# Performance work log

Measured on AMD Instinct MI355X. Metric: run time of the kernel, lower is better.

Reference implementation:

```python
import jax, jax.numpy as jnp
import numpy as np
import math

D_SINGLE, D_PAIR, H, PQ, PV = 384, 128, 12, 4, 8
DH = D_SINGLE // H
OUT_DIM = H * DH + H * PV * 4 + H * D_PAIR


def setup_inputs() -> dict:
    key = jax.random.key(0)
    ks = jax.random.split(key, 24)
    B, L = 1, 512
    inp = {
        'single': jax.random.normal(ks[0], (B, L, D_SINGLE), jnp.float32),
        'pair': jax.random.normal(ks[1], (B, L, L, D_PAIR), jnp.float32),
        'rot_mats': jax.random.normal(ks[2], (B, L, 3, 3), jnp.float32),
        'trans': jax.random.normal(ks[3], (B, L, 3), jnp.float32),
        'mask': jnp.ones((B, L), jnp.float32),
        'ln_w': jnp.ones((D_SINGLE,), jnp.float32),
        'ln_b': jnp.zeros((D_SINGLE,), jnp.float32),
        'Wq': jax.random.normal(ks[4], (D_SINGLE, H * DH), jnp.float32) * 0.02,
        'bq': jnp.zeros((H * DH,), jnp.float32),
        'Wk': jax.random.normal(ks[5], (D_SINGLE, H * DH), jnp.float32) * 0.02,
        'bk': jnp.zeros((H * DH,), jnp.float32),
        'Wv': jax.random.normal(ks[6], (D_SINGLE, H * DH), jnp.float32) * 0.02,
        'bv': jnp.zeros((H * DH,), jnp.float32),
        'Wqp': jax.random.normal(ks[7], (D_SINGLE, H * PQ * 3), jnp.float32) * 0.02,
        'bqp': jnp.zeros((H * PQ * 3,), jnp.float32),
        'Wkp': jax.random.normal(ks[8], (D_SINGLE, H * PQ * 3), jnp.float32) * 0.02,
        'bkp': jnp.zeros((H * PQ * 3,), jnp.float32),
        'Wvp': jax.random.normal(ks[9], (D_SINGLE, H * PV * 3), jnp.float32) * 0.02,
        'bvp': jnp.zeros((H * PV * 3,), jnp.float32),
        'Wpb': jax.random.normal(ks[10], (D_PAIR, H), jnp.float32) * 0.02,
        'bpb': jnp.zeros((H,), jnp.float32),
        'Wo': jax.random.normal(ks[11], (OUT_DIM, D_SINGLE), jnp.float32) * 0.02,
        'bo': jnp.zeros((D_SINGLE,), jnp.float32),
        'w_c': jnp.asarray(1.0 / math.sqrt(3.0), jnp.float32),
        'w_l': jnp.asarray(1.0 / 3.0, jnp.float32),
        'gamma_h': jnp.ones((H,), jnp.float32),
    }
    return inp


def _layer_norm(x, w, b, eps=1e-5):
    mu = jnp.mean(x, axis=-1, keepdims=True)
    var = jnp.mean((x - mu) ** 2, axis=-1, keepdims=True)
    return (x - mu) * jax.lax.rsqrt(var + eps) * w + b


def reference(single, pair, rot_mats, trans, mask, ln_w, ln_b, Wq, bq, Wk, bk, Wv, bv,
              Wqp, bqp, Wkp, bkp, Wvp, bvp, Wpb, bpb, Wo, bo, w_c, w_l, gamma_h):
    B, L, _ = single.shape
    sn = _layer_norm(single, ln_w, ln_b)
    q = (sn @ Wq + bq).reshape(B, L, H, DH)
    k = (sn @ Wk + bk).reshape(B, L, H, DH)
    v = (sn @ Wv + bv).reshape(B, L, H, DH)
    qp = (sn @ Wqp + bqp).reshape(B, L, H, PQ, 3)
    kp = (sn @ Wkp + bkp).reshape(B, L, H, PQ, 3)
    vp = (sn @ Wvp + bvp).reshape(B, L, H, PV, 3)

    t = trans[:, :, None, None, :]  # [B,L,1,1,3]
    qg = jnp.einsum('blij,blhpj->blhpi', rot_mats, qp) + t
    kg = jnp.einsum('blij,blhpj->blhpi', rot_mats, kp) + t
    vg = jnp.einsum('blij,blhpj->blhpi', rot_mats, vp) + t

    # sequence logits [B,H,L,L]
    seq_logits = jnp.einsum('bihd,bjhd->bhij', q, k) * w_c / math.sqrt(DH)

    # geometric logits: pairwise point distances [B,H,L,L]
    q_pts = jnp.transpose(qg, (0, 2, 1, 3, 4))  # [B,H,L,PQ,3]
    k_pts = jnp.transpose(kg, (0, 2, 1, 3, 4))
    diff = q_pts[:, :, :, None] - k_pts[:, :, None]  # [B,H,L,L,PQ,3]
    dist_sq = jnp.sum(diff ** 2, axis=-1)            # [B,H,L,L,PQ]
    geo_logits = -0.5 * jnp.sum(dist_sq, axis=-1) * gamma_h[None, :, None, None] * w_l

    pair_bias = jnp.transpose(pair @ Wpb + bpb, (0, 3, 1, 2))  # [B,H,L,L]
    logits = seq_logits + geo_logits + pair_bias

    mask_2d = (mask[:, :, None] * mask[:, None, :])[:, None]  # [B,1,L,L]
    logits = jnp.where(mask_2d > 0, logits, jnp.float32(-1e9))
    attn = jax.nn.softmax(logits, axis=-1)  # [B,H,L,L]

    # sequence aggregation -> [B,L,H,DH]
    seq_out = jnp.einsum('bhij,bjhd->bihd', attn, v).reshape(B, L, H * DH)

    # point aggregation -> local frame features
    pts_out = jnp.einsum('bhij,bjhpd->bihpd', attn, vg)  # [B,L,H,PV,3]
    pts_local = jnp.einsum('blji,blhpj->blhpi', rot_mats, pts_out - t)
    pts_norm = jnp.linalg.norm(pts_local, axis=-1, keepdims=True)
    pts_feat = jnp.concatenate([pts_norm, pts_local], axis=-1).reshape(B, L, H * PV * 4)

    # pair aggregation -> [B,L,H*D_PAIR]
    pair_out = jnp.einsum('bhij,bijd->bihd', attn, pair).reshape(B, L, H * D_PAIR)

    combined = jnp.concatenate([seq_out, pts_feat, pair_out], axis=-1)
    return combined @ Wo + bo
```

## Files before the change

### kernel.cpp

```cpp
#include <hip/hip_runtime.h>
#include <math.h>

#define LQ    512
#define DS    384
#define DPAIR 128
#define NH    12
#define NPP   1792
#define FE    48
#define TJC   64
#define NC    8

__global__ void k_concat_w(const float* __restrict__ Wq, const float* __restrict__ Wk,
                           const float* __restrict__ Wv, const float* __restrict__ Wqp,
                           const float* __restrict__ Wkp, const float* __restrict__ Wvp,
                           const float* __restrict__ bq, const float* __restrict__ bk,
                           const float* __restrict__ bv, const float* __restrict__ bqp,
                           const float* __restrict__ bkp, const float* __restrict__ bvp,
                           const float* __restrict__ Wpb,
                           float* __restrict__ Wcat, float* __restrict__ bcat,
                           float* __restrict__ WpbT) {
  int idx = blockIdx.x * 256 + threadIdx.x;
  const int total = DS * NPP;
  if (idx < total) {
    int k = idx / NPP, c = idx % NPP;
    float v = 0.f;
    if (c < 384)       v = Wq[k*384 + c];
    else if (c < 768)  v = Wk[k*384 + c-384];
    else if (c < 1152) v = Wv[k*384 + c-768];
    else if (c < 1296) v = Wqp[k*144 + c-1152];
    else if (c < 1440) v = Wkp[k*144 + c-1296];
    else if (c < 1728) v = Wvp[k*288 + c-1440];
    Wcat[idx] = v;
  } else if (idx < total + NPP) {
    int c = idx - total;
    float v = 0.f;
    if (c < 384)       v = bq[c];
    else if (c < 768)  v = bk[c-384];
    else if (c < 1152) v = bv[c-768];
    else if (c < 1296) v = bqp[c-1152];
    else if (c < 1440) v = bkp[c-1296];
    else if (c < 1728) v = bvp[c-1440];
    bcat[c] = v;
  } else if (idx < total + NPP + DPAIR*NH) {
    int e = idx - total - NPP;
    int k = e / NH, h = e % NH;
    WpbT[h*DPAIR + k] = Wpb[e];
  }
}

__global__ __launch_bounds__(128) void k_layernorm(const float* __restrict__ x,
                                                   const float* __restrict__ w,
                                                   const float* __restrict__ b,
                                                   float* __restrict__ y) {
  __shared__ float red[128];
  __shared__ float s_mu, s_rstd;
  int i = blockIdx.x, t = threadIdx.x;
  float v0 = x[i*DS + t], v1 = x[i*DS + t + 128], v2 = x[i*DS + t + 256];
  red[t] = v0 + v1 + v2; __syncthreads();
  for (int s = 64; s > 0; s >>= 1) { if (t < s) red[t] += red[t+s]; __syncthreads(); }
  if (t == 0) s_mu = red[0] * (1.f/384.f);
  __syncthreads();
  float mu = s_mu;
  float d0 = v0-mu, d1 = v1-mu, d2 = v2-mu;
  red[t] = d0*d0 + d1*d1 + d2*d2; __syncthreads();
  for (int s = 64; s > 0; s >>= 1) { if (t < s) red[t] += red[t+s]; __syncthreads(); }
  if (t == 0) s_rstd = rsqrtf(red[0] * (1.f/384.f) + 1e-5f);
  __syncthreads();
  float r = s_rstd;
  y[i*DS + t      ] = d0*r*w[t      ] + b[t      ];
  y[i*DS + t + 128] = d1*r*w[t + 128] + b[t + 128];
  y[i*DS + t + 256] = d2*r*w[t + 256] + b[t + 256];
}

__global__ __launch_bounds__(256) void k_gemm_nn(const float* __restrict__ A,
                                                 const float* __restrict__ B,
                                                 const float* __restrict__ bias,
                                                 float* __restrict__ C,
                                                 float* __restrict__ Cpart,
                                                 int M, int N, int K) {
  __shared__ float As[16*68];
  __shared__ float Bs[16*68];
  int t = threadIdx.x;
  int mg = t >> 4, ng = t & 15;
  int i0 = blockIdx.y * 64, j0 = blockIdx.x * 64;
  int KS = gridDim.z;
  int kper = K / KS;
  int kbeg = blockIdx.z * kper;
  float acc[4][4] = {};
  for (int k0 = kbeg; k0 < kbeg + kper; k0 += 16) {
    int e = t;
    #pragma unroll
    for (int s = 0; s < 4; s++, e += 256) {
      int m = e >> 4, k = e & 15;
      As[k*68 + m] = A[(size_t)(i0+m)*K + k0 + k];
      int k2 = e >> 6, n = e & 63;
      Bs[k2*68 + n] = B[(size_t)(k0+k2)*N + j0 + n];
    }
    __syncthreads();
    #pragma unroll
    for (int k = 0; k < 16; k++) {
      float4 av = *(const float4*)(As + k*68 + mg*4);
      float4 bv = *(const float4*)(Bs + k*68 + ng*4);
      float a[4] = {av.x, av.y, av.z, av.w};
      float b[4] = {bv.x, bv.y, bv.z, bv.w};
      #pragma unroll
      for (int y = 0; y < 4; y++)
        #pragma unroll
        for (int x = 0; x < 4; x++)
          acc[y][x] = fmaf(a[y], b[x], acc[y][x]);
    }
    __syncthreads();
  }
  if (KS == 1) {
    #pragma unroll
    for (int y = 0; y < 4; y++) {
      int m = i0 + mg*4 + y;
      #pragma unroll
      for (int x = 0; x < 4; x++) {
        int n = j0 + ng*4 + x;
        C[(size_t)m*N + n] = acc[y][x] + bias[n];
      }
    }
  } else {
    float* dst = Cpart + (size_t)blockIdx.z * M * N;
    #pragma unroll
    for (int y = 0; y < 4; y++) {
      int m = i0 + mg*4 + y;
      #pragma unroll
      for (int x = 0; x < 4; x++) {
        int n = j0 + ng*4 + x;
        dst[(size_t)m*N + n] = acc[y][x];
      }
    }
  }
}

__global__ void k_reduce_bias(const float* __restrict__ part, const float* __restrict__ bias,
                              float* __restrict__ out, int MN, int N, int KS) {
  int e = blockIdx.x * 256 + threadIdx.x;
  if (e >= MN) return;
  float s = bias[e % N];
  for (int z = 0; z < KS; z++) s += part[(size_t)z*MN + e];
  out[e] = s;
}

__global__ void k_rotfeat(const float* __restrict__ C1, const float* __restrict__ rot,
                          const float* __restrict__ trans, const float* __restrict__ gamma,
                          const float* __restrict__ w_c, const float* __restrict__ w_l,
                          float* __restrict__ Af, float* __restrict__ Bf,
                          float* __restrict__ vgb) {
  int idx = blockIdx.x * 256 + threadIdx.x;
  if (idx >= LQ*NH) return;
  int h = idx % NH, i = idx / NH;
  float R[9], tr[3];
  #pragma unroll
  for (int r = 0; r < 9; r++) R[r] = rot[(size_t)i*9 + r];
  #pragma unroll
  for (int r = 0; r < 3; r++) tr[r] = trans[(size_t)i*3 + r];

  float s  = w_c[0] * rsqrtf(32.f);
  float gp = gamma[h] * w_l[0];
  float* a  = Af + ((size_t)h*LQ + i)*FE;
  float* bb = Bf + ((size_t)h*LQ + i)*FE;
  const float* q = C1 + (size_t)i*NPP + h*32;
  const float* k = C1 + (size_t)i*NPP + 384 + h*32;
  #pragma unroll 8
  for (int d = 0; d < 32; d++) { a[d] = s*q[d]; bb[d] = k[d]; }

  const float* qp = C1 + (size_t)i*NPP + 1152 + h*12;
  const float* kp = C1 + (size_t)i*NPP + 1296 + h*12;
  float sq = 0.f, sk = 0.f;
  #pragma unroll
  for (int p = 0; p < 4; p++) {
    float x = qp[p*3], y = qp[p*3+1], z = qp[p*3+2];
    #pragma unroll
    for (int r = 0; r < 3; r++) {
      float g = fmaf(R[r*3],x, fmaf(R[r*3+1],y, fmaf(R[r*3+2],z, tr[r])));
      a[32 + p*3 + r] = gp*g;
      sq = fmaf(g,g,sq);
    }
    float xk = kp[p*3], yk = kp[p*3+1], zk = kp[p*3+2];
    #pragma unroll
    for (int r = 0; r < 3; r++) {
      float g = fmaf(R[r*3],xk, fmaf(R[r*3+1],yk, fmaf(R[r*3+2],zk, tr[r])));
      bb[32 + p*3 + r] = g;
      sk = fmaf(g,g,sk);
    }
  }
  a[44] = -0.5f*gp*sq; a[45] = 1.f; a[46] = 0.f; a[47] = 0.f;
  bb[44] = 1.f; bb[45] = -0.5f*gp*sk; bb[46] = 0.f; bb[47] = 0.f;

  const float* vp = C1 + (size_t)i*NPP + 1440 + h*24;
  float* vd = vgb + ((size_t)i*NH + h)*24;
  #pragma unroll
  for (int p = 0; p < 8; p++) {
    float x = vp[p*3], y = vp[p*3+1], z = vp[p*3+2];
    #pragma unroll
    for (int r = 0; r < 3; r++)
      vd[p*3 + r] = fmaf(R[r*3],x, fmaf(R[r*3+1],y, fmaf(R[r*3+2],z, tr[r])));
  }
}

__global__ __launch_bounds__(256) void k_logits_nt(const float* __restrict__ Af,
                                                   const float* __restrict__ Bf,
                                                   float* __restrict__ S) {
  __shared__ float As[48*68];
  __shared__ float Bs[48*68];
  int h = blockIdx.z;
  int i0 = blockIdx.y * 64, j0 = blockIdx.x * 64;
  int t = threadIdx.x;
  int mg = t >> 4, ng = t & 15;
  const float* Ah = Af + (size_t)h*LQ*FE;
  const float* Bh = Bf + (size_t)h*LQ*FE;
  for (int e = t; e < 64*48; e += 256) {
    int m = e / 48, k = e % 48;
    As[k*68 + m] = Ah[(size_t)(i0+m)*FE + k];
    Bs[k*68 + m] = Bh[(size_t)(j0+m)*FE + k];
  }
  __syncthreads();
  float acc[4][4] = {};
  #pragma unroll 8
  for (int k = 0; k < 48; k++) {
    float4 av = *(const float4*)(As + k*68 + mg*4);
    float4 bv = *(const float4*)(Bs + k*68 + ng*4);
    float a[4] = {av.x, av.y, av.z, av.w};
    float b[4] = {bv.x, bv.y, bv.z, bv.w};
    #pragma unroll
    for (int y = 0; y < 4; y++)
      #pragma unroll
      for (int x = 0; x < 4; x++)
        acc[y][x] = fmaf(a[y], b[x], acc[y][x]);
  }
  #pragma unroll
  for (int y = 0; y < 4; y++) {
    #pragma unroll
    for (int x = 0; x < 4; x++)
      S[((size_t)h*LQ + i0 + mg*4 + y)*LQ + j0 + ng*4 + x] = acc[y][x];
  }
}

__global__ __launch_bounds__(256, 2) void k_pair_chunk(
    const float* __restrict__ pair, const float* __restrict__ WpbT,
    const float* __restrict__ bpb, const float* __restrict__ mask,
    float* __restrict__ S, float* __restrict__ pairpart, float* __restrict__ msum) {
  __shared__ float tile[TJC*133];
  __shared__ float wt[NH*TJC];
  int i = blockIdx.x, c = blockIdx.y, t = threadIdx.x;
  int j0 = c*TJC;

  const float4* src = (const float4*)(pair + ((size_t)i*LQ + j0)*DPAIR);
  #pragma unroll
  for (int u = 0; u < 8; u++) {
    int e = t + u*256; int row = e >> 5, c4 = e & 31;
    *(float4*)&tile[row*133 + c4*4] = src[e];
  }

  int j = t & 63;
  int hg = __builtin_amdgcn_readfirstlane(t >> 6);
  int h0 = hg*3;
  float l[3];
  #pragma unroll
  for (int q = 0; q < 3; q++)
    l[q] = S[((size_t)(h0+q)*LQ + i)*LQ + j0 + j] + bpb[h0+q];
  bool dead = (mask[i] * mask[j0 + j] <= 0.f);
  __syncthreads();

  {
    const float* w0p = WpbT + (size_t)(h0+0)*DPAIR;
    const float* w1p = WpbT + (size_t)(h0+1)*DPAIR;
    const float* w2p = WpbT + (size_t)(h0+2)*DPAIR;
    float a0 = 0.f, a1 = 0.f, a2 = 0.f;
    #pragma unroll 8
    for (int k = 0; k < DPAIR; k += 4) {
      float4 pv = *(const float4*)&tile[j*133 + k];
      float4 w0 = *(const float4*)(w0p + k);
      float4 w1 = *(const float4*)(w1p + k);
      float4 w2 = *(const float4*)(w2p + k);
      a0 = fmaf(pv.x,w0.x, fmaf(pv.y,w0.y, fmaf(pv.z,w0.z, fmaf(pv.w,w0.w, a0))));
      a1 = fmaf(pv.x,w1.x, fmaf(pv.y,w1.y, fmaf(pv.z,w1.z, fmaf(pv.w,w1.w, a1))));
      a2 = fmaf(pv.x,w2.x, fmaf(pv.y,w2.y, fmaf(pv.z,w2.z, fmaf(pv.w,w2.w, a2))));
    }
    l[0] += a0; l[1] += a1; l[2] += a2;
    if (dead) { l[0] = -1e9f; l[1] = -1e9f; l[2] = -1e9f; }
  }

  #pragma unroll
  for (int q = 0; q < 3; q++) {
    float m = l[q];
    #pragma unroll
    for (int o = 32; o > 0; o >>= 1) m = fmaxf(m, __shfl_xor(m, o, 64));
    float w = __expf(l[q] - m);
    float sm = w;
    #pragma unroll
    for (int o = 32; o > 0; o >>= 1) sm += __shfl_xor(sm, o, 64);
    wt[(h0+q)*TJC + j] = w;
    S[((size_t)(h0+q)*LQ + i)*LQ + j0 + j] = w;
    if (j == 0) {
      float* dst = msum + (((size_t)i*NC + c)*NH + h0 + q)*2;
      dst[0] = m; dst[1] = sm;
    }
  }
  __syncthreads();

  int dg = t & 31, strip = t >> 5, jb = strip*8;
  float4 pv[8];
  #pragma unroll
  for (int q = 0; q < 8; q++) pv[q] = *(const float4*)&tile[(jb+q)*133 + dg*4];
  float4 acc[NH];
  #pragma unroll
  for (int h = 0; h < NH; h++) acc[h] = make_float4(0.f,0.f,0.f,0.f);
  #pragma unroll
  for (int h = 0; h < NH; h++) {
    float4 w0 = *(const float4*)&wt[h*TJC + jb];
    float4 w1 = *(const float4*)&wt[h*TJC + jb + 4];
    float wq[8] = {w0.x,w0.y,w0.z,w0.w,w1.x,w1.y,w1.z,w1.w};
    float4 a = acc[h];
    #pragma unroll
    for (int q = 0; q < 8; q++) {
      a.x = fmaf(wq[q], pv[q].x, a.x);
      a.y = fmaf(wq[q], pv[q].y, a.y);
      a.z = fmaf(wq[q], pv[q].z, a.z);
      a.w = fmaf(wq[q], pv[q].w, a.w);
    }
    acc[h] = a;
  }
  __syncthreads();

  float4* red4 = (float4*)tile;
  float4 tot[2];
  tot[0] = make_float4(0.f,0.f,0.f,0.f);
  tot[1] = make_float4(0.f,0.f,0.f,0.f);
  #pragma unroll
  for (int half = 0; half < 2; half++) {
    if ((strip >> 2) == half) {
      #pragma unroll
      for (int h = 0; h < NH; h++)
        red4[(((strip & 3)*NH) + h)*32 + dg] = acc[h];
    }
    __syncthreads();
    for (int e = t, u = 0; e < NH*32; e += 256, u++) {
      int rh = e >> 5, rd = e & 31;
      #pragma unroll
      for (int s4 = 0; s4 < 4; s4++) {
        float4 v = red4[((s4*NH) + rh)*32 + rd];
        tot[u].x += v.x; tot[u].y += v.y; tot[u].z += v.z; tot[u].w += v.w;
      }
    }
    __syncthreads();
  }
  for (int e = t, u = 0; e < NH*32; e += 256, u++) {
    int rh = e >> 5, rd = e & 31;
    *(float4*)&pairpart[(((size_t)i*NC + c)*NH + rh)*DPAIR + rd*4] = tot[u];
  }
}

__global__ __launch_bounds__(384) void k_scs_pairout(
    const float* __restrict__ msum, const float* __restrict__ pairpart,
    float* __restrict__ scs_g, float* __restrict__ comb) {
  __shared__ float scs[NH*NC];
  int i = blockIdx.x, t = threadIdx.x;
  if (t < NH) {
    float m = -3.0e38f;
    float mc[NC], sc_[NC];
    #pragma unroll
    for (int c = 0; c < NC; c++) {
      const float* p = msum + (((size_t)i*NC + c)*NH + t)*2;
      mc[c] = p[0]; sc_[c] = p[1];
      m = fmaxf(m, mc[c]);
    }
    float s = 0.f;
    #pragma unroll
    for (int c = 0; c < NC; c++) s += sc_[c] * __expf(mc[c] - m);
    float inv = 1.f / s;
    #pragma unroll
    for (int c = 0; c < NC; c++) {
      float v = __expf(mc[c] - m) * inv;
      scs[t*NC + c] = v;
      scs_g[((size_t)i*NH + t)*NC + c] = v;
    }
  }
  __syncthreads();
  int h = t >> 5, d = t & 31;
  float4 tot = make_float4(0.f,0.f,0.f,0.f);
  #pragma unroll
  for (int c = 0; c < NC; c++) {
    float sc = scs[h*NC + c];
    float4 v = *(const float4*)&pairpart[(((size_t)i*NC + c)*NH + h)*DPAIR + d*4];
    tot.x = fmaf(v.x, sc, tot.x); tot.y = fmaf(v.y, sc, tot.y);
    tot.z = fmaf(v.z, sc, tot.z); tot.w = fmaf(v.w, sc, tot.w);
  }
  *(float4*)&comb[(size_t)i*2304 + 768 + h*DPAIR + d*4] = tot;
}

__global__ __launch_bounds__(256) void k_attn_v(const float* __restrict__ attn,
                                                const float* __restrict__ C1,
                                                const float* __restrict__ vg,
                                                const float* __restrict__ scs,
                                                float* __restrict__ psum) {
  __shared__ float As[64*68];
  __shared__ float Vs[64*68];
  int i0 = blockIdx.x * 64;
  int h = blockIdx.y;
  int z = blockIdx.z;
  int t = threadIdx.x;
  int mg = t >> 4, ng = t & 15;
  float acc[4][4] = {};
  for (int k0 = z*128; k0 < z*128 + 128; k0 += 64) {
    int c = k0 >> 6;
    __syncthreads();
    for (int e = t; e < 64*64; e += 256) {
      int m = e >> 6, j = e & 63;
      float sc = scs[((size_t)(i0+m)*NH + h)*NC + c];
      As[j*68 + m] = attn[((size_t)h*LQ + i0 + m)*LQ + k0 + j] * sc;
    }
    for (int e = t; e < 64*64; e += 256) {
      int j = e >> 6, cc = e & 63;
      float v = 0.f;
      if (cc < 32)      v = C1[(size_t)(k0+j)*NPP + 768 + h*32 + cc];
      else if (cc < 56) v = vg[((size_t)(k0+j)*NH + h)*24 + (cc-32)];
      Vs[j*68 + cc] = v;
    }
    __syncthreads();
    #pragma unroll 4
    for (int j = 0; j < 64; j++) {
      float4 av = *(const float4*)(As + j*68 + mg*4);
      float4 bv = *(const float4*)(Vs + j*68 + ng*4);
      float a[4] = {av.x, av.y, av.z, av.w};
      float b[4] = {bv.x, bv.y, bv.z, bv.w};
      #pragma unroll
      for (int y = 0; y < 4; y++)
        #pragma unroll
        for (int x = 0; x < 4; x++)
          acc[y][x] = fmaf(a[y], b[x], acc[y][x]);
    }
  }
  #pragma unroll
  for (int y = 0; y < 4; y++) {
    int i = i0 + mg*4 + y;
    #pragma unroll
    for (int x = 0; x < 4; x++) {
      int n = ng*4 + x;
      psum[(((size_t)z*LQ + i)*NH + h)*64 + n] = acc[y][x];
    }
  }
}

__global__ void k_avpts(const float* __restrict__ psum, const float* __restrict__ rot,
                        const float* __restrict__ trans, float* __restrict__ comb) {
  int idx = blockIdx.x * 256 + threadIdx.x;
  if (idx >= LQ*NH*40) return;
  int w = idx % 40; int ih = idx / 40; int h = ih % NH; int i = ih / NH;
  size_t base = ((size_t)i*NH + h)*64;
  if (w < 32) {
    float s = 0.f;
    for (int z = 0; z < 4; z++) s += psum[(size_t)z*LQ*NH*64 + base + w];
    comb[(size_t)i*2304 + h*32 + w] = s;
  } else {
    int p = w - 32;
    float g[3];
    #pragma unroll
    for (int r = 0; r < 3; r++) {
      int n = 32 + p*3 + r;
      float s = 0.f;
      for (int z = 0; z < 4; z++) s += psum[(size_t)z*LQ*NH*64 + base + n];
      g[r] = s;
    }
    const float* R = rot + (size_t)i*9;
    const float* tr = trans + (size_t)i*3;
    float x = g[0]-tr[0], y = g[1]-tr[1], z = g[2]-tr[2];
    float lx = fmaf(R[0],x, fmaf(R[3],y, R[6]*z));
    float ly = fmaf(R[1],x, fmaf(R[4],y, R[7]*z));
    float lz = fmaf(R[2],x, fmaf(R[5],y, R[8]*z));
    float nrm = sqrtf(fmaf(lx,lx, fmaf(ly,ly, lz*lz)));
    float* dst = comb + (size_t)i*2304 + 384 + (h*8 + p)*4;
    dst[0] = nrm; dst[1] = lx; dst[2] = ly; dst[3] = lz;
  }
}

extern "C" void kernel_launch(void* const* d_in, const int* in_sizes, int n_in,
                              void* d_out, int out_size, void* d_ws, size_t ws_size,
                              hipStream_t stream) {
  const float* single = (const float*)d_in[0];
  const float* pair   = (const float*)d_in[1];
  const float* rot    = (const float*)d_in[2];
  const float* trans  = (const float*)d_in[3];
  const float* mask   = (const float*)d_in[4];
  const float* ln_w   = (const float*)d_in[5];
  const float* ln_b   = (const float*)d_in[6];
  const float* Wq     = (const float*)d_in[7];
  const float* bq     = (const float*)d_in[8];
  const float* Wk     = (const float*)d_in[9];
  const float* bk     = (const float*)d_in[10];
  const float* Wv     = (const float*)d_in[11];
  const float* bv     = (const float*)d_in[12];
  const float* Wqp    = (const float*)d_in[13];
  const float* bqp    = (const float*)d_in[14];
  const float* Wkp    = (const float*)d_in[15];
  const float* bkp    = (const float*)d_in[16];
  const float* Wvp    = (const float*)d_in[17];
  const float* bvp    = (const float*)d_in[18];
  const float* Wpb    = (const float*)d_in[19];
  const float* bpb    = (const float*)d_in[20];
  const float* Wo     = (const float*)d_in[21];
  const float* bo     = (const float*)d_in[22];
  const float* w_c    = (const float*)d_in[23];
  const float* w_l    = (const float*)d_in[24];
  const float* gamma  = (const float*)d_in[25];
  float* out = (float*)d_out;

  float* p = (float*)d_ws;
  auto alloc = [&](size_t n) { float* r = p; p += n; return r; };
  float* Wcat    = alloc((size_t)DS*NPP);
  float* bcat    = alloc(NPP);
  float* WpbT    = alloc((size_t)NH*DPAIR);
  float* sn      = alloc((size_t)LQ*DS);
  float* C1      = alloc((size_t)LQ*NPP);
  float* vgb     = alloc((size_t)LQ*NH*24);
  float* Af      = alloc((size_t)NH*LQ*FE);
  float* Bf      = alloc((size_t)NH*LQ*FE);
  float* S       = alloc((size_t)NH*LQ*LQ);
  float* pairpart= alloc((size_t)LQ*NC*NH*DPAIR);
  float* msum    = alloc((size_t)LQ*NC*NH*2);
  float* scs_g   = alloc((size_t)LQ*NH*NC);
  float* comb    = alloc((size_t)LQ*2304);
  float* scratch = alloc((size_t)2*LQ*NPP);

  k_concat_w<<<dim3((DS*NPP + NPP + DPAIR*NH + 255)/256), 256, 0, stream>>>(
      Wq, Wk, Wv, Wqp, Wkp, Wvp, bq, bk, bv, bqp, bkp, bvp, Wpb, Wcat, bcat, WpbT);
  k_layernorm<<<dim3(LQ), 128, 0, stream>>>(single, ln_w, ln_b, sn);
  k_gemm_nn<<<dim3(NPP/64, LQ/64, 2), 256, 0, stream>>>(sn, Wcat, nullptr, nullptr, scratch, LQ, NPP, DS);
  k_reduce_bias<<<dim3((LQ*NPP + 255)/256), 256, 0, stream>>>(scratch, bcat, C1, LQ*NPP, NPP, 2);
  k_rotfeat<<<dim3((LQ*NH + 255)/256), 256, 0, stream>>>(C1, rot, trans, gamma, w_c, w_l, Af, Bf, vgb);
  k_logits_nt<<<dim3(LQ/64, LQ/64, NH), 256, 0, stream>>>(Af, Bf, S);
  k_pair_chunk<<<dim3(LQ, NC), 256, 0, stream>>>(pair, WpbT, bpb, mask, S, pairpart, msum);
  k_scs_pairout<<<dim3(LQ), 384, 0, stream>>>(msum, pairpart, scs_g, comb);
  k_attn_v<<<dim3(LQ/64, NH, 4), 256, 0, stream>>>(S, C1, vgb, scs_g, scratch);
  k_avpts<<<dim3((LQ*NH*40 + 255)/256), 256, 0, stream>>>(scratch, rot, trans, comb);
  k_gemm_nn<<<dim3(DS/64, LQ/64, 8), 256, 0, stream>>>(comb, Wo, nullptr, nullptr, scratch, LQ, DS, 2304);
  k_reduce_bias<<<dim3((LQ*DS + 255)/256), 256, 0, stream>>>(scratch, bo, out, LQ*DS, DS, 8);
}
```

Measured before the change: 377.1 us.

## Run projection and output GEMMs on MFMA with split-bf16 emulated fp32

```diff
diff --git a/kernel.cpp b/kernel.cpp
--- a/kernel.cpp
+++ b/kernel.cpp
@@ -10,48 +10,116 @@
 #define TJC   64
 #define NC    8
 
-__global__ void k_concat_w(const float* __restrict__ Wq, const float* __restrict__ Wk,
-                           const float* __restrict__ Wv, const float* __restrict__ Wqp,
-                           const float* __restrict__ Wkp, const float* __restrict__ Wvp,
-                           const float* __restrict__ bq, const float* __restrict__ bk,
-                           const float* __restrict__ bv, const float* __restrict__ bqp,
-                           const float* __restrict__ bkp, const float* __restrict__ bvp,
-                           const float* __restrict__ Wpb,
-                           float* __restrict__ Wcat, float* __restrict__ bcat,
-                           float* __restrict__ WpbT) {
-  int idx = blockIdx.x * 256 + threadIdx.x;
-  const int total = DS * NPP;
-  if (idx < total) {
-    int k = idx / NPP, c = idx % NPP;
-    float v = 0.f;
-    if (c < 384)       v = Wq[k*384 + c];
-    else if (c < 768)  v = Wk[k*384 + c-384];
-    else if (c < 1152) v = Wv[k*384 + c-768];
-    else if (c < 1296) v = Wqp[k*144 + c-1152];
-    else if (c < 1440) v = Wkp[k*144 + c-1296];
-    else if (c < 1728) v = Wvp[k*288 + c-1440];
-    Wcat[idx] = v;
-  } else if (idx < total + NPP) {
-    int c = idx - total;
-    float v = 0.f;
-    if (c < 384)       v = bq[c];
-    else if (c < 768)  v = bk[c-384];
-    else if (c < 1152) v = bv[c-768];
-    else if (c < 1296) v = bqp[c-1152];
-    else if (c < 1440) v = bkp[c-1296];
-    else if (c < 1728) v = bvp[c-1440];
-    bcat[c] = v;
-  } else if (idx < total + NPP + DPAIR*NH) {
-    int e = idx - total - NPP;
-    int k = e / NH, h = e % NH;
-    WpbT[h*DPAIR + k] = Wpb[e];
-  }
+typedef unsigned short u16;
+typedef unsigned int   u32;
+typedef __attribute__((ext_vector_type(8))) short bf16x8;
+typedef __attribute__((ext_vector_type(4))) float f32x4;
+
+__device__ inline u16 bf16_rne(float x) {
+  u32 u = __float_as_uint(x);
+  u32 r = (u + 0x7FFFu + ((u >> 16) & 1u)) >> 16;
+  return (u16)r;
+}
+__device__ inline void split_bf16(float x, u16& h, u16& l) {
+  u16 hb = bf16_rne(x);
+  float hf = __uint_as_float(((u32)hb) << 16);
+  h = hb;
+  l = bf16_rne(x - hf);
+}
+
+__global__ __launch_bounds__(256) void k_concat_wT(
+    const float* __restrict__ Wq, const float* __restrict__ Wk,
+    const float* __restrict__ Wv, const float* __restrict__ Wqp,
+    const float* __restrict__ Wkp, const float* __restrict__ Wvp,
+    const float* __restrict__ bq, const float* __restrict__ bk,
+    const float* __restrict__ bv, const float* __restrict__ bqp,
+    const float* __restrict__ bkp, const float* __restrict__ bvp,
+    const float* __restrict__ Wpb,
+    u16* __restrict__ Wth, u16* __restrict__ Wtl,
+    float* __restrict__ bcat, float* __restrict__ WpbT) {
+  int blk = blockIdx.x, t = threadIdx.x;
+  if (blk < 168) {
+    __shared__ u16 hi[64][66], lo[64][66];
+    int kb = blk / 28, cb = blk % 28;
+    int k0 = kb * 64, c0 = cb * 64;
+    for (int e = t; e < 4096; e += 256) {
+      int rr = e >> 6, cc = e & 63;
+      int k = k0 + rr, c = c0 + cc;
+      float v = 0.f;
+      if (c < 384)       v = Wq[k*384 + c];
+      else if (c < 768)  v = Wk[k*384 + c-384];
+      else if (c < 1152) v = Wv[k*384 + c-768];
+      else if (c < 1296) v = Wqp[k*144 + c-1152];
+      else if (c < 1440) v = Wkp[k*144 + c-1296];
+      else if (c < 1728) v = Wvp[k*288 + c-1440];
+      u16 h_, l_; split_bf16(v, h_, l_);
+      hi[rr][cc] = h_; lo[rr][cc] = l_;
+    }
+    __syncthreads();
+    for (int e = t; e < 4096; e += 256) {
+      int cc = e >> 6, kk = e & 63;
+      Wth[(size_t)(c0+cc)*DS + k0 + kk] = hi[kk][cc];
+      Wtl[(size_t)(c0+cc)*DS + k0 + kk] = lo[kk][cc];
+    }
+  } else {
+    for (int e = t; e < NPP + NH*DPAIR; e += 256) {
+      if (e < NPP) {
+        int c = e;
+        float v = 0.f;
+        if (c < 384)       v = bq[c];
+        else if (c < 768)  v = bk[c-384];
+        else if (c < 1152) v = bv[c-768];
+        else if (c < 1296) v = bqp[c-1152];
+        else if (c < 1440) v = bkp[c-1296];
+        else if (c < 1728) v = bvp[c-1440];
+        bcat[c] = v;
+      } else {
+        int e2 = e - NPP;
+        int k = e2 / NH, h = e2 % NH;
+        WpbT[h*DPAIR + k] = Wpb[e2];
+      }
+    }
+  }
+}
+
+__global__ __launch_bounds__(256) void k_transpose_split(
+    const float* __restrict__ src, u16* __restrict__ dh, u16* __restrict__ dl,
+    int R, int Cc) {
+  __shared__ u16 hi[64][66], lo[64][66];
+  int r0 = blockIdx.x * 64, c0 = blockIdx.y * 64, t = threadIdx.x;
+  for (int e = t; e < 4096; e += 256) {
+    int rr = e >> 6, cc = e & 63;
+    float v = src[(size_t)(r0+rr)*Cc + c0 + cc];
+    u16 h_, l_; split_bf16(v, h_, l_);
+    hi[rr][cc] = h_; lo[rr][cc] = l_;
+  }
+  __syncthreads();
+  for (int e = t; e < 4096; e += 256) {
+    int cc = e >> 6, rr = e & 63;
+    dh[(size_t)(c0+cc)*R + r0 + rr] = hi[rr][cc];
+    dl[(size_t)(c0+cc)*R + r0 + rr] = lo[rr][cc];
+  }
+}
+
+__global__ void k_split4(const float* __restrict__ src, u16* __restrict__ h,
+                         u16* __restrict__ l, int n4) {
+  int e = blockIdx.x * 256 + threadIdx.x;
+  if (e >= n4) return;
+  float4 v = ((const float4*)src)[e];
+  u16 h0,l0,h1,l1,h2,l2,h3,l3;
+  split_bf16(v.x, h0, l0); split_bf16(v.y, h1, l1);
+  split_bf16(v.z, h2, l2); split_bf16(v.w, h3, l3);
+  uint2 hp, lp;
+  hp.x = (u32)h0 | ((u32)h1 << 16); hp.y = (u32)h2 | ((u32)h3 << 16);
+  lp.x = (u32)l0 | ((u32)l1 << 16); lp.y = (u32)l2 | ((u32)l3 << 16);
+  ((uint2*)h)[e] = hp; ((uint2*)l)[e] = lp;
 }
 
 __global__ __launch_bounds__(128) void k_layernorm(const float* __restrict__ x,
                                                    const float* __restrict__ w,
                                                    const float* __restrict__ b,
-                                                   float* __restrict__ y) {
+                                                   u16* __restrict__ yh,
+                                                   u16* __restrict__ yl) {
   __shared__ float red[128];
   __shared__ float s_mu, s_rstd;
   int i = blockIdx.x, t = threadIdx.x;
@@ -67,70 +135,84 @@
   if (t == 0) s_rstd = rsqrtf(red[0] * (1.f/384.f) + 1e-5f);
   __syncthreads();
   float r = s_rstd;
-  y[i*DS + t      ] = d0*r*w[t      ] + b[t      ];
-  y[i*DS + t + 128] = d1*r*w[t + 128] + b[t + 128];
-  y[i*DS + t + 256] = d2*r*w[t + 256] + b[t + 256];
-}
-
-__global__ __launch_bounds__(256) void k_gemm_nn(const float* __restrict__ A,
-                                                 const float* __restrict__ B,
-                                                 const float* __restrict__ bias,
-                                                 float* __restrict__ C,
-                                                 float* __restrict__ Cpart,
-                                                 int M, int N, int K) {
-  __shared__ float As[16*68];
-  __shared__ float Bs[16*68];
+  float y0 = d0*r*w[t      ] + b[t      ];
+  float y1 = d1*r*w[t + 128] + b[t + 128];
+  float y2 = d2*r*w[t + 256] + b[t + 256];
+  u16 h_, l_;
+  split_bf16(y0, h_, l_); yh[i*DS + t      ] = h_; yl[i*DS + t      ] = l_;
+  split_bf16(y1, h_, l_); yh[i*DS + t + 128] = h_; yl[i*DS + t + 128] = l_;
+  split_bf16(y2, h_, l_); yh[i*DS + t + 256] = h_; yl[i*DS + t + 256] = l_;
+}
+
+__global__ __launch_bounds__(256) void k_gemm_mfma(
+    const u16* __restrict__ Ah, const u16* __restrict__ Al,
+    const u16* __restrict__ Bth, const u16* __restrict__ Btl,
+    const float* __restrict__ bias, float* __restrict__ C,
+    float* __restrict__ Cpart, int M, int N, int K) {
   int t = threadIdx.x;
-  int mg = t >> 4, ng = t & 15;
-  int i0 = blockIdx.y * 64, j0 = blockIdx.x * 64;
+  int lane = t & 63, wave = t >> 6;
+  int wr = wave >> 1, wc = wave & 1;
+  int i0 = blockIdx.y * 64 + wr * 32;
+  int j0 = blockIdx.x * 64 + wc * 32;
   int KS = gridDim.z;
   int kper = K / KS;
-  int kbeg = blockIdx.z * kper;
-  float acc[4][4] = {};
-  for (int k0 = kbeg; k0 < kbeg + kper; k0 += 16) {
-    int e = t;
-    #pragma unroll
-    for (int s = 0; s < 4; s++, e += 256) {
-      int m = e >> 4, k = e & 15;
-      As[k*68 + m] = A[(size_t)(i0+m)*K + k0 + k];
-      int k2 = e >> 6, n = e & 63;
-      Bs[k2*68 + n] = B[(size_t)(k0+k2)*N + j0 + n];
-    }
-    __syncthreads();
-    #pragma unroll
-    for (int k = 0; k < 16; k++) {
-      float4 av = *(const float4*)(As + k*68 + mg*4);
-      float4 bv = *(const float4*)(Bs + k*68 + ng*4);
-      float a[4] = {av.x, av.y, av.z, av.w};
-      float b[4] = {bv.x, bv.y, bv.z, bv.w};
-      #pragma unroll
-      for (int y = 0; y < 4; y++)
-        #pragma unroll
-        for (int x = 0; x < 4; x++)
-          acc[y][x] = fmaf(a[y], b[x], acc[y][x]);
-    }
-    __syncthreads();
-  }
+  size_t kbeg = (size_t)blockIdx.z * kper;
+  int lr = lane & 15, lk = (lane >> 4) << 3;
+
+  const u16* a0h = Ah  + (size_t)(i0 + lr) * K + kbeg + lk;
+  const u16* a1h = a0h + (size_t)16 * K;
+  const u16* a0l = Al  + (size_t)(i0 + lr) * K + kbeg + lk;
+  const u16* a1l = a0l + (size_t)16 * K;
+  const u16* b0h = Bth + (size_t)(j0 + lr) * K + kbeg + lk;
+  const u16* b1h = b0h + (size_t)16 * K;
+  const u16* b0l = Btl + (size_t)(j0 + lr) * K + kbeg + lk;
+  const u16* b1l = b0l + (size_t)16 * K;
+
+  f32x4 c00 = {0.f,0.f,0.f,0.f}, c01 = c00, c10 = c00, c11 = c00;
+  for (int k = 0; k < kper; k += 32) {
+    bf16x8 A0h = *(const bf16x8*)(a0h + k);
+    bf16x8 A1h = *(const bf16x8*)(a1h + k);
+    bf16x8 B0h = *(const bf16x8*)(b0h + k);
+    bf16x8 B1h = *(const bf16x8*)(b1h + k);
+    bf16x8 A0l = *(const bf16x8*)(a0l + k);
+    bf16x8 A1l = *(const bf16x8*)(a1l + k);
+    bf16x8 B0l = *(const bf16x8*)(b0l + k);
+    bf16x8 B1l = *(const bf16x8*)(b1l + k);
+    c00 = __builtin_amdgcn_mfma_f32_16x16x32_bf16(A0h, B0h, c00, 0, 0, 0);
+    c01 = __builtin_amdgcn_mfma_f32_16x16x32_bf16(A0h, B1h, c01, 0, 0, 0);
+    c10 = __builtin_amdgcn_mfma_f32_16x16x32_bf16(A1h, B0h, c10, 0, 0, 0);
+    c11 = __builtin_amdgcn_mfma_f32_16x16x32_bf16(A1h, B1h, c11, 0, 0, 0);
+    c00 = __builtin_amdgcn_mfma_f32_16x16x32_bf16(A0h, B0l, c00, 0, 0, 0);
+    c01 = __builtin_amdgcn_mfma_f32_16x16x32_bf16(A0h, B1l, c01, 0, 0, 0);
+    c10 = __builtin_amdgcn_mfma_f32_16x16x32_bf16(A1h, B0l, c10, 0, 0, 0);
+    c11 = __builtin_amdgcn_mfma_f32_16x16x32_bf16(A1h, B1l, c11, 0, 0, 0);
+    c00 = __builtin_amdgcn_mfma_f32_16x16x32_bf16(A0l, B0h, c00, 0, 0, 0);
+    c01 = __builtin_amdgcn_mfma_f32_16x16x32_bf16(A0l, B1h, c01, 0, 0, 0);
+    c10 = __builtin_amdgcn_mfma_f32_16x16x32_bf16(A1l, B0h, c10, 0, 0, 0);
+    c11 = __builtin_amdgcn_mfma_f32_16x16x32_bf16(A1l, B1h, c11, 0, 0, 0);
+  }
+
+  int orow = (lane >> 4) << 2;
+  int col0 = j0 + lr, col1 = j0 + 16 + lr;
   if (KS == 1) {
-    #pragma unroll
-    for (int y = 0; y < 4; y++) {
-      int m = i0 + mg*4 + y;
-      #pragma unroll
-      for (int x = 0; x < 4; x++) {
-        int n = j0 + ng*4 + x;
-        C[(size_t)m*N + n] = acc[y][x] + bias[n];
-      }
+    float bb0 = bias[col0], bb1 = bias[col1];
+    #pragma unroll
+    for (int r = 0; r < 4; r++) {
+      int row0 = i0 + orow + r, row1 = row0 + 16;
+      C[(size_t)row0*N + col0] = c00[r] + bb0;
+      C[(size_t)row0*N + col1] = c01[r] + bb1;
+      C[(size_t)row1*N + col0] = c10[r] + bb0;
+      C[(size_t)row1*N + col1] = c11[r] + bb1;
     }
   } else {
     float* dst = Cpart + (size_t)blockIdx.z * M * N;
     #pragma unroll
-    for (int y = 0; y < 4; y++) {
-      int m = i0 + mg*4 + y;
-      #pragma unroll
-      for (int x = 0; x < 4; x++) {
-        int n = j0 + ng*4 + x;
-        dst[(size_t)m*N + n] = acc[y][x];
-      }
+    for (int r = 0; r < 4; r++) {
+      int row0 = i0 + orow + r, row1 = row0 + 16;
+      dst[(size_t)row0*N + col0] = c00[r];
+      dst[(size_t)row0*N + col1] = c01[r];
+      dst[(size_t)row1*N + col0] = c10[r];
+      dst[(size_t)row1*N + col1] = c11[r];
     }
   }
 }
@@ -210,12 +292,12 @@
   int i0 = blockIdx.y * 64, j0 = blockIdx.x * 64;
   int t = threadIdx.x;
   int mg = t >> 4, ng = t & 15;
-  const float* Ah = Af + (size_t)h*LQ*FE;
-  const float* Bh = Bf + (size_t)h*LQ*FE;
+  const float* Ahp = Af + (size_t)h*LQ*FE;
+  const float* Bhp = Bf + (size_t)h*LQ*FE;
   for (int e = t; e < 64*48; e += 256) {
     int m = e / 48, k = e % 48;
-    As[k*68 + m] = Ah[(size_t)(i0+m)*FE + k];
-    Bs[k*68 + m] = Bh[(size_t)(j0+m)*FE + k];
+    As[k*68 + m] = Ahp[(size_t)(i0+m)*FE + k];
+    Bs[k*68 + m] = Bhp[(size_t)(j0+m)*FE + k];
   }
   __syncthreads();
   float acc[4][4] = {};
@@ -510,10 +592,16 @@
 
   float* p = (float*)d_ws;
   auto alloc = [&](size_t n) { float* r = p; p += n; return r; };
-  float* Wcat    = alloc((size_t)DS*NPP);
+  u16* WcatTh = (u16*)alloc((size_t)NPP*DS/2);
+  u16* WcatTl = (u16*)alloc((size_t)NPP*DS/2);
+  u16* snh    = (u16*)alloc((size_t)LQ*DS/2);
+  u16* snl    = (u16*)alloc((size_t)LQ*DS/2);
+  u16* WoTh   = (u16*)alloc((size_t)DS*2304/2);
+  u16* WoTl   = (u16*)alloc((size_t)DS*2304/2);
+  u16* combh  = (u16*)alloc((size_t)LQ*2304/2);
+  u16* combl  = (u16*)alloc((size_t)LQ*2304/2);
   float* bcat    = alloc(NPP);
   float* WpbT    = alloc((size_t)NH*DPAIR);
-  float* sn      = alloc((size_t)LQ*DS);
   float* C1      = alloc((size_t)LQ*NPP);
   float* vgb     = alloc((size_t)LQ*NH*24);
   float* Af      = alloc((size_t)NH*LQ*FE);
@@ -525,17 +613,21 @@
   float* comb    = alloc((size_t)LQ*2304);
   float* scratch = alloc((size_t)2*LQ*NPP);
 
-  k_concat_w<<<dim3((DS*NPP + NPP + DPAIR*NH + 255)/256), 256, 0, stream>>>(
-      Wq, Wk, Wv, Wqp, Wkp, Wvp, bq, bk, bv, bqp, bkp, bvp, Wpb, Wcat, bcat, WpbT);
-  k_layernorm<<<dim3(LQ), 128, 0, stream>>>(single, ln_w, ln_b, sn);
-  k_gemm_nn<<<dim3(NPP/64, LQ/64, 2), 256, 0, stream>>>(sn, Wcat, nullptr, nullptr, scratch, LQ, NPP, DS);
-  k_reduce_bias<<<dim3((LQ*NPP + 255)/256), 256, 0, stream>>>(scratch, bcat, C1, LQ*NPP, NPP, 2);
+  k_concat_wT<<<dim3(169), 256, 0, stream>>>(
+      Wq, Wk, Wv, Wqp, Wkp, Wvp, bq, bk, bv, bqp, bkp, bvp, Wpb,
+      WcatTh, WcatTl, bcat, WpbT);
+  k_transpose_split<<<dim3(2304/64, DS/64), 256, 0, stream>>>(Wo, WoTh, WoTl, 2304, DS);
+  k_layernorm<<<dim3(LQ), 128, 0, stream>>>(single, ln_w, ln_b, snh, snl);
+  k_gemm_mfma<<<dim3(NPP/64, LQ/64, 1), 256, 0, stream>>>(
+      snh, snl, WcatTh, WcatTl, bcat, C1, nullptr, LQ, NPP, DS);
   k_rotfeat<<<dim3((LQ*NH + 255)/256), 256, 0, stream>>>(C1, rot, trans, gamma, w_c, w_l, Af, Bf, vgb);
   k_logits_nt<<<dim3(LQ/64, LQ/64, NH), 256, 0, stream>>>(Af, Bf, S);
   k_pair_chunk<<<dim3(LQ, NC), 256, 0, stream>>>(pair, WpbT, bpb, mask, S, pairpart, msum);
   k_scs_pairout<<<dim3(LQ), 384, 0, stream>>>(msum, pairpart, scs_g, comb);
   k_attn_v<<<dim3(LQ/64, NH, 4), 256, 0, stream>>>(S, C1, vgb, scs_g, scratch);
   k_avpts<<<dim3((LQ*NH*40 + 255)/256), 256, 0, stream>>>(scratch, rot, trans, comb);
-  k_gemm_nn<<<dim3(DS/64, LQ/64, 8), 256, 0, stream>>>(comb, Wo, nullptr, nullptr, scratch, LQ, DS, 2304);
+  k_split4<<<dim3((LQ*2304/4 + 255)/256), 256, 0, stream>>>(comb, combh, combl, LQ*2304/4);
+  k_gemm_mfma<<<dim3(DS/64, LQ/64, 8), 256, 0, stream>>>(
+      combh, combl, WoTh, WoTl, nullptr, nullptr, scratch, LQ, DS, 2304);
   k_reduce_bias<<<dim3((LQ*DS + 255)/256), 256, 0, stream>>>(scratch, bo, out, LQ*DS, DS, 8);
 }
```

New measurement: 384.2 us. No clear change (+1.9%).
